# Performance work log

Measured on AMD Instinct MI355X. Metric: run time of the kernel, lower is better.

Reference implementation:

```python
import jax, jax.numpy as jnp
import numpy as np

N = 20000      # nodes
E = 320000     # edges (avg degree 16)
D = 128        # emb_dim
L = 5          # num_layer
NV = 119       # node vocab (atom types)
EV = 5         # edge vocab (bond types)
BN_EPS = 1e-5


def setup_inputs() -> dict:
    key = jax.random.key(0)
    ks = jax.random.split(key, 8)
    s = 0.1
    return {
        "x": jax.random.randint(ks[0], (N,), 0, NV),
        "edge_index": jax.random.randint(ks[1], (2, E), 0, N),
        "edge_attr": jax.random.randint(ks[2], (E,), 0, EV),
        "node_emb1": jax.random.normal(ks[3], (NV, D), jnp.float32) * s,
        "node_emb2": jax.random.normal(ks[4], (NV, D), jnp.float32) * s,
        "edge_emb": jax.random.normal(ks[5], (2, L, EV, D), jnp.float32) * s,
        "eps": jnp.zeros((2, L), jnp.float32),
        "W": jax.random.normal(ks[6], (2, L, D, D), jnp.float32) / np.sqrt(D).astype(np.float32),
        "b": jnp.zeros((2, L, D), jnp.float32),
        "bn_gamma": jnp.ones((2, L, D), jnp.float32),
        "bn_beta": jnp.zeros((2, L, D), jnp.float32),
        "cross_unit": jnp.full((L, 2, 2), 0.5, jnp.float32),
    }


def gin_conv(h, src, dst, eattr, edge_tab, eps, W, b):
    # message: relu(x_j + edge_embedding), aggregated by add at target nodes
    msg = jax.nn.relu(h[src] + edge_tab[eattr])            # [E, D]
    agg = jax.ops.segment_sum(msg, dst, num_segments=h.shape[0])  # [N, D]
    return ((1.0 + eps) * h + agg) @ W.T + b               # mlp = single Linear


def batch_norm(h, gamma, beta):
    # training-mode BatchNorm1d over the node dimension (biased variance)
    mu = h.mean(axis=0)
    var = h.var(axis=0)
    return (h - mu) * jax.lax.rsqrt(var + BN_EPS) * gamma + beta


def reference(x, edge_index, edge_attr, node_emb1, node_emb2, edge_emb, eps, W, b,
              bn_gamma, bn_beta, cross_unit):
    src, dst = edge_index[0], edge_index[1]
    h1 = node_emb1[x]   # NodeEncoder tower 1
    h2 = node_emb2[x]   # NodeEncoder tower 2
    for l in range(L):
        a1 = gin_conv(h1, src, dst, edge_attr, edge_emb[0, l], eps[0, l], W[0, l], b[0, l])
        a1 = batch_norm(a1, bn_gamma[0, l], bn_beta[0, l])
        a2 = gin_conv(h2, src, dst, edge_attr, edge_emb[1, l], eps[1, l], W[1, l], b[1, l])
        a2 = batch_norm(a2, bn_gamma[1, l], bn_beta[1, l])
        if l < L - 1:
            a1 = jax.nn.relu(a1)
            a2 = jax.nn.relu(a2)
        # dropout: identity (eval mode / deterministic reference)
        # cross-stitch; note h_2 uses the UPDATED h_1 (faithful to source)
        c = cross_unit[l]
        n1 = c[0, 0] * a1 + c[0, 1] * a2
        n2 = c[1, 0] * n1 + c[1, 1] * a2
        h1, h2 = n1, n2
    return (h1, h2)  # JK == 'last'
```

## Files before the change

kernel.cpp:

```cpp
#include <hip/hip_runtime.h>

#define NN 20000
#define EE 320000
#define DD 128
#define LL 5
#define EVV 5
#define BNEPS 1e-5f
#define NB 313
#define EMB_BLOCKS 2500
#define CVT_BLOCKS 160
#define CNT_BLOCKS 1250

typedef __attribute__((ext_vector_type(8))) short bf8_t;
typedef __attribute__((ext_vector_type(4))) float f4_t;
typedef __attribute__((ext_vector_type(8))) unsigned short us8;

__device__ inline unsigned short f2bf(float f) {
    union { float f; unsigned u; } v;
    v.f = f;
    unsigned r = v.u + 0x7fffu + ((v.u >> 16) & 1u);
    return (unsigned short)(r >> 16);
}
__device__ inline float bf2f(unsigned short h) {
    union { unsigned u; float f; } v;
    v.u = ((unsigned)h) << 16;
    return v.f;
}
__device__ inline float4 bf2f4(ushort4 u) {
    float4 f;
    f.x = bf2f(u.x); f.y = bf2f(u.y); f.z = bf2f(u.z); f.w = bf2f(u.w);
    return f;
}
__device__ inline float4 add4(float4 a, float4 b) {
    float4 r;
    r.x = a.x + b.x; r.y = a.y + b.y; r.z = a.z + b.z; r.w = a.w + b.w;
    return r;
}

__device__ inline void xform4(float4 v1, float4 v2,
                              float4 s1, float4 t1, float4 s2, float4 t2,
                              float c00, float c01, float c10, float c11,
                              int dorelu, float4& n1, float4& n2) {
    float x1, x2, m1, m2;
#define XE(f)                                                    \
    x1 = v1.f * s1.f + t1.f;                                     \
    x2 = v2.f * s2.f + t2.f;                                     \
    x1 = dorelu ? fmaxf(x1, 0.f) : x1;                           \
    x2 = dorelu ? fmaxf(x2, 0.f) : x2;                           \
    m1 = c00 * x1 + c01 * x2;                                    \
    m2 = c10 * m1 + c11 * x2;                                    \
    n1.f = m1;                                                   \
    n2.f = m2;
    XE(x) XE(y) XE(z) XE(w)
#undef XE
}

__device__ inline void bn_coeffs(const float* __restrict__ statsL,
                                 const float* __restrict__ gall,
                                 const float* __restrict__ btall,
                                 int pl, int c,
                                 float4& s1, float4& t1, float4& s2, float4& t2) {
    const float inv = 1.0f / (float)NN;
    int ch = c * 4;
#define BNC(tw, sv, tv)                                                       \
    {                                                                         \
        const float* gp = gall + (size_t)((tw) * LL + pl) * DD + ch;          \
        const float* bp = btall + (size_t)((tw) * LL + pl) * DD + ch;         \
        float r[4];                                                           \
        _Pragma("unroll") for (int j = 0; j < 4; j++) {                       \
            float sum = statsL[(tw) * 256 + ch + j];                          \
            float sq = statsL[(tw) * 256 + 128 + ch + j];                     \
            float mu = sum * inv;                                             \
            float var = sq * inv - mu * mu;                                   \
            float rs = rsqrtf(var + BNEPS);                                   \
            float sc = rs * gp[j];                                            \
            r[j] = sc;                                                        \
            ((float*)&tv)[j] = bp[j] - mu * sc;                               \
        }                                                                     \
        sv.x = r[0]; sv.y = r[1]; sv.z = r[2]; sv.w = r[3];                   \
    }
    BNC(0, s1, t1)
    BNC(1, s2, t2)
#undef BNC
}

__device__ inline ushort4 hi4(float4 v) {
    ushort4 h;
    h.x = f2bf(v.x); h.y = f2bf(v.y); h.z = f2bf(v.z); h.w = f2bf(v.w);
    return h;
}
__device__ inline ushort4 lo4(float4 v, ushort4 h) {
    ushort4 l;
    l.x = f2bf(v.x - bf2f(h.x)); l.y = f2bf(v.y - bf2f(h.y));
    l.z = f2bf(v.z - bf2f(h.z)); l.w = f2bf(v.w - bf2f(h.w));
    return l;
}


__global__ __launch_bounds__(256) void prep_kernel(
    const int* __restrict__ x,
    const float4* __restrict__ e1, const float4* __restrict__ e2,
    ushort4* __restrict__ yh, ushort4* __restrict__ yl,
    const float4* __restrict__ Wall,
    ushort4* __restrict__ Wbh, ushort4* __restrict__ Wbl,
    const int* __restrict__ dst, int* __restrict__ deg,
    float* __restrict__ stats,
    const float* __restrict__ etab, unsigned short* __restrict__ etb2) {
    int bid = blockIdx.x;
    int tid = threadIdx.x;
    if (bid < EMB_BLOCKS) {
        int idx = bid * 256 + tid;
        int r = idx >> 5, c = idx & 31;
        int v = x[r];
        float4 w1 = e1[v * 32 + c];
        float4 w2 = e2[v * 32 + c];
        ushort4 h = hi4(w1);
        yh[(size_t)r * 64 + c] = h;
        yl[(size_t)r * 64 + c] = lo4(w1, h);
        h = hi4(w2);
        yh[(size_t)r * 64 + 32 + c] = h;
        yl[(size_t)r * 64 + 32 + c] = lo4(w2, h);
    } else if (bid < EMB_BLOCKS + CVT_BLOCKS) {
        int i = (bid - EMB_BLOCKS) * 256 + tid;
        float4 w = Wall[i];
        ushort4 oh = hi4(w);
        Wbh[i] = oh;
        Wbl[i] = lo4(w, oh);
    } else if (bid < EMB_BLOCKS + CVT_BLOCKS + CNT_BLOCKS) {
        int e = (bid - EMB_BLOCKS - CVT_BLOCKS) * 256 + tid;
        atomicAdd(&deg[dst[e]], 1);
    } else {
#pragma unroll
        for (int i = 0; i < 10; i++) stats[i * 256 + tid] = 0.f;
        for (int idx = tid; idx < 2 * LL * EVV * DD; idx += 256) {
            int ch = idx & 127;
            int tw = (idx >> 7) & 1;
            int la = idx >> 8;
            int a = la % EVV;
            int l = la / EVV;
            etb2[idx] = f2bf(etab[((size_t)(tw * LL + l) * EVV + a) * DD + ch]);
        }
    }
}


__global__ __launch_bounds__(1024) void scan_kernel(const int* __restrict__ deg,
                                                    int* __restrict__ offs,
                                                    int* __restrict__ pos) {
    __shared__ int wsum[16];
    int t = threadIdx.x;
    int lane = t & 63, wv = t >> 6;
    int base = t * 20;
    int loc[20];
    int s = 0;
#pragma unroll
    for (int i = 0; i < 20; i++) {
        int j = base + i;
        int d = (j < NN) ? deg[j] : 0;
        loc[i] = d;
        s += d;
    }
    int incl = s;
#pragma unroll
    for (int o = 1; o < 64; o <<= 1) {
        int v = __shfl_up(incl, o, 64);
        if (lane >= o) incl += v;
    }
    if (lane == 63) wsum[wv] = incl;
    __syncthreads();
    if (t < 16) {
        int v = wsum[t];
        int iv = v;
#pragma unroll
        for (int o = 1; o < 16; o <<= 1) {
            int u = __shfl_up(iv, o, 64);
            if (t >= o) iv += u;
        }
        wsum[t] = iv - v;
    }
    __syncthreads();
    int run = wsum[wv] + (incl - s);
#pragma unroll
    for (int i = 0; i < 20; i++) {
        int j = base + i;
        if (j < NN) {
            offs[j] = run;
            pos[j] = run;
            run += loc[i];
        }
    }
}

__global__ __launch_bounds__(256) void scatter_kernel(const int* __restrict__ src,
                                                      const int* __restrict__ dst,
                                                      const int* __restrict__ eattr,
                                                      int* __restrict__ pos,
                                                      int2* __restrict__ erec) {
    int e = blockIdx.x * 256 + threadIdx.x;
    if (e < EE) {
        int d = dst[e];
        int p = atomicAdd(&pos[d], 1);
        erec[p] = make_int2(src[e], eattr[e]);
    }
}


__global__ __launch_bounds__(256) void xform_kernel(
    const ushort4* __restrict__ yh, const ushort4* __restrict__ yl,
    ushort4* __restrict__ hph, ushort4* __restrict__ hpl,
    const float* __restrict__ statsL,
    const float* __restrict__ gall, const float* __restrict__ btall,
    const float* __restrict__ crossp, int pl) {
    int idx = blockIdx.x * 256 + threadIdx.x;
    int r = idx >> 5, c = idx & 31;
    float4 s1, t1, s2, t2;
    bn_coeffs(statsL, gall, btall, pl, c, s1, t1, s2, t2);
    float c00 = crossp[0], c01 = crossp[1], c10 = crossp[2], c11 = crossp[3];
    float4 v1 = add4(bf2f4(yh[(size_t)r * 64 + c]), bf2f4(yl[(size_t)r * 64 + c]));
    float4 v2 = add4(bf2f4(yh[(size_t)r * 64 + 32 + c]), bf2f4(yl[(size_t)r * 64 + 32 + c]));
    float4 n1, n2;
    xform4(v1, v2, s1, t1, s2, t2, c00, c01, c10, c11, 1, n1, n2);
    ushort4 h = hi4(n1);
    hph[(size_t)r * 64 + c] = h;
    hpl[(size_t)r * 64 + c] = lo4(n1, h);
    h = hi4(n2);
    hph[(size_t)r * 64 + 32 + c] = h;
    hpl[(size_t)r * 64 + 32 + c] = lo4(n2, h);
}


__global__ __launch_bounds__(256) void aggregate_kernel(
    const us8* __restrict__ hph, const us8* __restrict__ hpl,
    const us8* __restrict__ etb2, int layer,
    const int* __restrict__ offs, const int* __restrict__ deg,
    const int2* __restrict__ erec, const float* __restrict__ epsall,
    us8* __restrict__ uo8) {
    int tid = threadIdx.x;
    int node = blockIdx.x * 4 + (tid >> 6);
    int lane = tid & 63;
    int slot = lane >> 5;
    int c = lane & 31;
    const us8* et = etb2 + (size_t)layer * EVV * 32;

    int off = offs[node];
    int dg = deg[node];
    float a[8];
#pragma unroll
    for (int k = 0; k < 8; k++) a[k] = 0.f;

    int i = 0;
    for (; i + 8 <= dg; i += 8) {
        int2 r0 = erec[off + i + slot];
        int2 r1 = erec[off + i + 2 + slot];
        int2 r2 = erec[off + i + 4 + slot];
        int2 r3 = erec[off + i + 6 + slot];
        us8 h0 = hph[(size_t)r0.x * 32 + c];
        us8 h1 = hph[(size_t)r1.x * 32 + c];
        us8 h2 = hph[(size_t)r2.x * 32 + c];
        us8 h3 = hph[(size_t)r3.x * 32 + c];
        us8 e0 = et[r0.y * 32 + c];
        us8 e1 = et[r1.y * 32 + c];
        us8 e2 = et[r2.y * 32 + c];
        us8 e3 = et[r3.y * 32 + c];
#pragma unroll
        for (int k = 0; k < 8; k++) {
            a[k] += fmaxf(bf2f(h0[k]) + bf2f(e0[k]), 0.f);
            a[k] += fmaxf(bf2f(h1[k]) + bf2f(e1[k]), 0.f);
            a[k] += fmaxf(bf2f(h2[k]) + bf2f(e2[k]), 0.f);
            a[k] += fmaxf(bf2f(h3[k]) + bf2f(e3[k]), 0.f);
        }
    }
    for (; i < dg; i += 2) {
        int j = i + slot;
        bool valid = j < dg;
        int e = off + (valid ? j : 0);
        int2 r = erec[e];
        us8 h = hph[(size_t)r.x * 32 + c];
        us8 ev = et[r.y * 32 + c];
        if (valid) {
#pragma unroll
            for (int k = 0; k < 8; k++) a[k] += fmaxf(bf2f(h[k]) + bf2f(ev[k]), 0.f);
        }
    }

#pragma unroll
    for (int k = 0; k < 8; k++) a[k] += __shfl_xor(a[k], 32, 64);

    us8 sh = hph[(size_t)node * 32 + c];
    us8 sl = hpl[(size_t)node * 32 + c];
    float ep = 1.0f + epsall[(c >> 4) * LL + layer];
    us8 uh, ul;
#pragma unroll
    for (int k = 0; k < 8; k++) {
        float u = ep * (bf2f(sh[k]) + bf2f(sl[k])) + a[k];
        unsigned short h = f2bf(u);
        uh[k] = h;
        ul[k] = f2bf(u - bf2f(h));
    }
    uo8[(size_t)node * 64 + slot * 32 + c] = slot ? ul : uh;
}


__global__ __launch_bounds__(256) void gemm_mfma_kernel(
    const unsigned short* __restrict__ ubuf,
    const unsigned short* __restrict__ Wbh, const unsigned short* __restrict__ Wbl,
    const float* __restrict__ ball, int layer,
    unsigned short* __restrict__ yh, unsigned short* __restrict__ yl,
    float* __restrict__ statsL) {
    __shared__ float accS[64 * 4 * 33];
    __shared__ float sP[2][4][DD];
    int tid = threadIdx.x;
    int tower = blockIdx.y;
    const bf8_t* Wh8 = (const bf8_t*)(Wbh + (size_t)(tower * LL + layer) * DD * DD);
    const bf8_t* Wl8 = (const bf8_t*)(Wbl + (size_t)(tower * LL + layer) * DD * DD);
    const float* bias = ball + (size_t)(tower * LL + layer) * DD;
    const bf8_t* u8 = (const bf8_t*)ubuf;

    int wave = tid >> 6, lane = tid & 63;
    int quad = lane >> 4, m = lane & 15;
    int row_base = blockIdx.x * 64 + wave * 16;

    f4_t acc[8];
#pragma unroll
    for (int nt = 0; nt < 8; nt++) {
        acc[nt][0] = 0.f; acc[nt][1] = 0.f; acc[nt][2] = 0.f; acc[nt][3] = 0.f;
    }

    int aidx = (row_base + m) * 64 + tower * 16;
#pragma unroll
    for (int kt = 0; kt < 4; kt++) {
        bf8_t ah = u8[aidx + kt * 4 + quad];
        bf8_t al = u8[aidx + 32 + kt * 4 + quad];
#pragma unroll
        for (int nt = 0; nt < 8; nt++) {
            bf8_t bh = Wh8[(nt * 16 + m) * 16 + kt * 4 + quad];
            bf8_t bl = Wl8[(nt * 16 + m) * 16 + kt * 4 + quad];
            acc[nt] = __builtin_amdgcn_mfma_f32_16x16x32_bf16(ah, bh, acc[nt], 0, 0, 0);
            acc[nt] = __builtin_amdgcn_mfma_f32_16x16x32_bf16(al, bh, acc[nt], 0, 0, 0);
            acc[nt] = __builtin_amdgcn_mfma_f32_16x16x32_bf16(ah, bl, acc[nt], 0, 0, 0);
        }
    }

#pragma unroll
    for (int nt = 0; nt < 8; nt++) {
        int col = nt * 16 + m;
        float bv = bias[col];
        int cg = col >> 5, kk = col & 31;
        float s = 0.f, q = 0.f;
#pragma unroll
        for (int r = 0; r < 4; r++) {
            int lrow = wave * 16 + quad * 4 + r;
            int row = blockIdx.x * 64 + lrow;
            float v = acc[nt][r] + bv;
            accS[(lrow * 4 + cg) * 33 + kk] = v;
            if (row < NN) { s += v; q += v * v; }
        }
        s += __shfl_xor(s, 16, 64); s += __shfl_xor(s, 32, 64);
        q += __shfl_xor(q, 16, 64); q += __shfl_xor(q, 32, 64);
        if (quad == 0) {
            sP[0][wave][col] = s;
            sP[1][wave][col] = q;
        }
    }
    __syncthreads();

    {
        int lrow = tid >> 2, cg = tid & 3;
        int grow = blockIdx.x * 64 + lrow;
        if (grow < NN) {
            const float* srcp = &accS[(lrow * 4 + cg) * 33];
            us8* yhp = (us8*)yh;
            us8* ylp = (us8*)yl;
            size_t base = (size_t)grow * 32 + tower * 16 + cg * 4;
#pragma unroll
            for (int j = 0; j < 4; j++) {
                us8 hv, lv;
#pragma unroll
                for (int k = 0; k < 8; k++) {
                    float v = srcp[j * 8 + k];
                    unsigned short h = f2bf(v);
                    hv[k] = h;
                    lv[k] = f2bf(v - bf2f(h));
                }
                yhp[base + j] = hv;
                ylp[base + j] = lv;
            }
        }
    }

    int ch = tid & 127, sq = tid >> 7;
    float v = sP[sq][0][ch] + sP[sq][1][ch] + sP[sq][2][ch] + sP[sq][3][ch];
    atomicAdd(&statsL[tower * 256 + tid], v);
}


__global__ __launch_bounds__(256) void bn_final_kernel(
    const ushort4* __restrict__ yh, const ushort4* __restrict__ yl,
    float4* __restrict__ o1, float4* __restrict__ o2,
    const float* __restrict__ statsL,
    const float* __restrict__ gall, const float* __restrict__ btall,
    const float* __restrict__ crossp) {
    int idx = blockIdx.x * 256 + threadIdx.x;
    int r = idx >> 5, c = idx & 31;
    float4 s1, t1, s2, t2;
    bn_coeffs(statsL, gall, btall, LL - 1, c, s1, t1, s2, t2);
    float c00 = crossp[0], c01 = crossp[1], c10 = crossp[2], c11 = crossp[3];
    float4 v1 = add4(bf2f4(yh[(size_t)r * 64 + c]), bf2f4(yl[(size_t)r * 64 + c]));
    float4 v2 = add4(bf2f4(yh[(size_t)r * 64 + 32 + c]), bf2f4(yl[(size_t)r * 64 + 32 + c]));
    float4 n1, n2;
    xform4(v1, v2, s1, t1, s2, t2, c00, c01, c10, c11, 0, n1, n2);
    o1[(size_t)r * 32 + c] = n1;
    o2[(size_t)r * 32 + c] = n2;
}


extern "C" void kernel_launch(void* const* d_in, const int* in_sizes, int n_in,
                              void* d_out, int out_size, void* d_ws, size_t ws_size,
                              hipStream_t stream) {
    const int* x = (const int*)d_in[0];
    const int* eidx = (const int*)d_in[1];
    const int* eattr = (const int*)d_in[2];
    const float* emb1 = (const float*)d_in[3];
    const float* emb2 = (const float*)d_in[4];
    const float* etab = (const float*)d_in[5];
    const float* epsv = (const float*)d_in[6];
    const float* Wall = (const float*)d_in[7];
    const float* ball = (const float*)d_in[8];
    const float* gall = (const float*)d_in[9];
    const float* btall = (const float*)d_in[10];
    const float* cross = (const float*)d_in[11];
    float* out = (float*)d_out;

    const size_t ND = (size_t)NN * DD;
    char* p = (char*)d_ws;
    unsigned short* yh = (unsigned short*)p;   p += (size_t)NN * 256 * 2;
    unsigned short* yl = (unsigned short*)p;   p += (size_t)NN * 256 * 2;
    unsigned short* hph = (unsigned short*)p;  p += (size_t)NN * 256 * 2;
    unsigned short* hpl = (unsigned short*)p;  p += (size_t)NN * 256 * 2;
    unsigned short* ubuf = (unsigned short*)p; p += (size_t)NN * 512 * 2;
    unsigned short* Wbh = (unsigned short*)p;  p += (size_t)2 * LL * DD * DD * 2;
    unsigned short* Wbl = (unsigned short*)p;  p += (size_t)2 * LL * DD * DD * 2;
    unsigned short* etb2 = (unsigned short*)p; p += (size_t)2 * LL * EVV * DD * 2;
    int* deg = (int*)p;               p += (size_t)NN * 4;
    int* offs = (int*)p;              p += (size_t)NN * 4;
    int* pos = (int*)p;               p += (size_t)NN * 4;
    int2* erec = (int2*)p;            p += (size_t)EE * 8;
    float* stats = (float*)p;         p += (size_t)LL * 512 * 4;

    const int* src = eidx;
    const int* dst = eidx + EE;

    hipMemsetAsync(deg, 0, (size_t)NN * 4, stream);
    prep_kernel<<<EMB_BLOCKS + CVT_BLOCKS + CNT_BLOCKS + 1, 256, 0, stream>>>(
        x, (const float4*)emb1, (const float4*)emb2,
        (ushort4*)yh, (ushort4*)yl,
        (const float4*)Wall, (ushort4*)Wbh, (ushort4*)Wbl, dst, deg, stats,
        etab, etb2);
    scan_kernel<<<1, 1024, 0, stream>>>(deg, offs, pos);
    scatter_kernel<<<EE / 256, 256, 0, stream>>>(src, dst, eattr, pos, erec);

    for (int l = 0; l < LL; l++) {
        const unsigned short* hsrc_h = yh;
        const unsigned short* hsrc_l = yl;
        if (l > 0) {
            xform_kernel<<<(NN * 32) / 256, 256, 0, stream>>>(
                (const ushort4*)yh, (const ushort4*)yl,
                (ushort4*)hph, (ushort4*)hpl,
                stats + (size_t)(l - 1) * 512, gall, btall,
                cross + (l - 1) * 4, l - 1);
            hsrc_h = hph;
            hsrc_l = hpl;
        }
        aggregate_kernel<<<NN / 4, 256, 0, stream>>>(
            (const us8*)hsrc_h, (const us8*)hsrc_l, (const us8*)etb2, l,
            offs, deg, erec, epsv, (us8*)ubuf);
        dim3 g(NB, 2);
        gemm_mfma_kernel<<<g, 256, 0, stream>>>(ubuf, Wbh, Wbl, ball, l, yh, yl,
                                                stats + (size_t)l * 512);
    }
    bn_final_kernel<<<(NN * 32) / 256, 256, 0, stream>>>(
        (const ushort4*)yh, (const ushort4*)yl, (float4*)out, (float4*)(out + ND),
        stats + (size_t)(LL - 1) * 512, gall, btall, cross + (LL - 1) * 4);
}
```

Measured before the change: 504.5 us.

## Fuse neighbor aggregation into MFMA GEMM via shared-memory staging

Merges the aggregation kernel and the split-bf16 GEMM kernel into one 512-thread kernel. Each block aggregates 64 nodes into an XOR-swizzled shared-memory tile, then eight waves run the MFMA GEMM for both towers and write outputs and BN statistics. This removes the global ubuf round trip and one launch per layer. The cost is only 313 blocks for the gather-heavy aggregation phase, which reduces the parallelism available to hide memory latency, plus more shared memory per block. Separate embedding buffers are added so the fused kernel can write yh/yl while layer 0 reads its input from eh/el.

```diff
diff --git a/kernel.cpp b/kernel.cpp
--- a/kernel.cpp
+++ b/kernel.cpp
@@ -6,7 +6,7 @@
 #define LL 5
 #define EVV 5
 #define BNEPS 1e-5f
-#define NB 313
+#define FB 313
 #define EMB_BLOCKS 2500
 #define CVT_BLOCKS 160
 #define CNT_BLOCKS 1250
@@ -100,7 +100,7 @@
 __global__ __launch_bounds__(256) void prep_kernel(
     const int* __restrict__ x,
     const float4* __restrict__ e1, const float4* __restrict__ e2,
-    ushort4* __restrict__ yh, ushort4* __restrict__ yl,
+    ushort4* __restrict__ eh, ushort4* __restrict__ el,
     const float4* __restrict__ Wall,
     ushort4* __restrict__ Wbh, ushort4* __restrict__ Wbl,
     const int* __restrict__ dst, int* __restrict__ deg,
@@ -115,11 +115,11 @@
         float4 w1 = e1[v * 32 + c];
         float4 w2 = e2[v * 32 + c];
         ushort4 h = hi4(w1);
-        yh[(size_t)r * 64 + c] = h;
-        yl[(size_t)r * 64 + c] = lo4(w1, h);
+        eh[(size_t)r * 64 + c] = h;
+        el[(size_t)r * 64 + c] = lo4(w1, h);
         h = hi4(w2);
-        yh[(size_t)r * 64 + 32 + c] = h;
-        yl[(size_t)r * 64 + 32 + c] = lo4(w2, h);
+        eh[(size_t)r * 64 + 32 + c] = h;
+        el[(size_t)r * 64 + 32 + c] = lo4(w2, h);
     } else if (bid < EMB_BLOCKS + CVT_BLOCKS) {
         int i = (bid - EMB_BLOCKS) * 256 + tid;
         float4 w = Wall[i];
@@ -229,108 +229,114 @@
 }
 
 
-__global__ __launch_bounds__(256) void aggregate_kernel(
+__global__ __launch_bounds__(512, 4) void agg_gemm_kernel(
     const us8* __restrict__ hph, const us8* __restrict__ hpl,
     const us8* __restrict__ etb2, int layer,
     const int* __restrict__ offs, const int* __restrict__ deg,
     const int2* __restrict__ erec, const float* __restrict__ epsall,
-    us8* __restrict__ uo8) {
-    int tid = threadIdx.x;
-    int node = blockIdx.x * 4 + (tid >> 6);
-    int lane = tid & 63;
-    int slot = lane >> 5;
-    int c = lane & 31;
-    const us8* et = etb2 + (size_t)layer * EVV * 32;
-
-    int off = offs[node];
-    int dg = deg[node];
-    float a[8];
-#pragma unroll
-    for (int k = 0; k < 8; k++) a[k] = 0.f;
-
-    int i = 0;
-    for (; i + 8 <= dg; i += 8) {
-        int2 r0 = erec[off + i + slot];
-        int2 r1 = erec[off + i + 2 + slot];
-        int2 r2 = erec[off + i + 4 + slot];
-        int2 r3 = erec[off + i + 6 + slot];
-        us8 h0 = hph[(size_t)r0.x * 32 + c];
-        us8 h1 = hph[(size_t)r1.x * 32 + c];
-        us8 h2 = hph[(size_t)r2.x * 32 + c];
-        us8 h3 = hph[(size_t)r3.x * 32 + c];
-        us8 e0 = et[r0.y * 32 + c];
-        us8 e1 = et[r1.y * 32 + c];
-        us8 e2 = et[r2.y * 32 + c];
-        us8 e3 = et[r3.y * 32 + c];
-#pragma unroll
-        for (int k = 0; k < 8; k++) {
-            a[k] += fmaxf(bf2f(h0[k]) + bf2f(e0[k]), 0.f);
-            a[k] += fmaxf(bf2f(h1[k]) + bf2f(e1[k]), 0.f);
-            a[k] += fmaxf(bf2f(h2[k]) + bf2f(e2[k]), 0.f);
-            a[k] += fmaxf(bf2f(h3[k]) + bf2f(e3[k]), 0.f);
-        }
-    }
-    for (; i < dg; i += 2) {
-        int j = i + slot;
-        bool valid = j < dg;
-        int e = off + (valid ? j : 0);
-        int2 r = erec[e];
-        us8 h = hph[(size_t)r.x * 32 + c];
-        us8 ev = et[r.y * 32 + c];
-        if (valid) {
-#pragma unroll
-            for (int k = 0; k < 8; k++) a[k] += fmaxf(bf2f(h[k]) + bf2f(ev[k]), 0.f);
-        }
-    }
-
-#pragma unroll
-    for (int k = 0; k < 8; k++) a[k] += __shfl_xor(a[k], 32, 64);
-
-    us8 sh = hph[(size_t)node * 32 + c];
-    us8 sl = hpl[(size_t)node * 32 + c];
-    float ep = 1.0f + epsall[(c >> 4) * LL + layer];
-    us8 uh, ul;
-#pragma unroll
-    for (int k = 0; k < 8; k++) {
-        float u = ep * (bf2f(sh[k]) + bf2f(sl[k])) + a[k];
-        unsigned short h = f2bf(u);
-        uh[k] = h;
-        ul[k] = f2bf(u - bf2f(h));
-    }
-    uo8[(size_t)node * 64 + slot * 32 + c] = slot ? ul : uh;
-}
-
-
-__global__ __launch_bounds__(256) void gemm_mfma_kernel(
-    const unsigned short* __restrict__ ubuf,
     const unsigned short* __restrict__ Wbh, const unsigned short* __restrict__ Wbl,
-    const float* __restrict__ ball, int layer,
+    const float* __restrict__ ball,
     unsigned short* __restrict__ yh, unsigned short* __restrict__ yl,
     float* __restrict__ statsL) {
-    __shared__ float accS[64 * 4 * 33];
-    __shared__ float sP[2][4][DD];
+    __shared__ float accS[2 * 64 * 4 * 33];
+    __shared__ float sP[2][2][4][DD];
+    us8* uS = (us8*)accS;
+
     int tid = threadIdx.x;
-    int tower = blockIdx.y;
+    int w = tid >> 6, lane = tid & 63;
+
+    {
+        int slot = lane >> 5;
+        int c = lane & 31;
+        const us8* et = etb2 + (size_t)layer * EVV * 32;
+        float ep = 1.0f + epsall[(c >> 4) * LL + layer];
+#pragma unroll 1
+        for (int rnd = 0; rnd < 8; rnd++) {
+            int row = w * 8 + rnd;
+            int node = blockIdx.x * 64 + row;
+            us8 outv;
+            if (node < NN) {
+                int off = offs[node];
+                int dg = deg[node];
+                float a[8];
+#pragma unroll
+                for (int k = 0; k < 8; k++) a[k] = 0.f;
+                int i = 0;
+                for (; i + 8 <= dg; i += 8) {
+                    int2 r0 = erec[off + i + slot];
+                    int2 r1 = erec[off + i + 2 + slot];
+                    int2 r2 = erec[off + i + 4 + slot];
+                    int2 r3 = erec[off + i + 6 + slot];
+                    us8 h0 = hph[(size_t)r0.x * 32 + c];
+                    us8 h1 = hph[(size_t)r1.x * 32 + c];
+                    us8 h2 = hph[(size_t)r2.x * 32 + c];
+                    us8 h3 = hph[(size_t)r3.x * 32 + c];
+                    us8 e0 = et[r0.y * 32 + c];
+                    us8 e1 = et[r1.y * 32 + c];
+                    us8 e2 = et[r2.y * 32 + c];
+                    us8 e3 = et[r3.y * 32 + c];
+#pragma unroll
+                    for (int k = 0; k < 8; k++) {
+                        a[k] += fmaxf(bf2f(h0[k]) + bf2f(e0[k]), 0.f);
+                        a[k] += fmaxf(bf2f(h1[k]) + bf2f(e1[k]), 0.f);
+                        a[k] += fmaxf(bf2f(h2[k]) + bf2f(e2[k]), 0.f);
+                        a[k] += fmaxf(bf2f(h3[k]) + bf2f(e3[k]), 0.f);
+                    }
+                }
+                for (; i < dg; i += 2) {
+                    int j = i + slot;
+                    bool valid = j < dg;
+                    int e = off + (valid ? j : 0);
+                    int2 r = erec[e];
+                    us8 h = hph[(size_t)r.x * 32 + c];
+                    us8 ev = et[r.y * 32 + c];
+                    if (valid) {
+#pragma unroll
+                        for (int k = 0; k < 8; k++)
+                            a[k] += fmaxf(bf2f(h[k]) + bf2f(ev[k]), 0.f);
+                    }
+                }
+#pragma unroll
+                for (int k = 0; k < 8; k++) a[k] += __shfl_xor(a[k], 32, 64);
+                us8 sh = hph[(size_t)node * 32 + c];
+                us8 sl = hpl[(size_t)node * 32 + c];
+                us8 uh, ul;
+#pragma unroll
+                for (int k = 0; k < 8; k++) {
+                    float u = ep * (bf2f(sh[k]) + bf2f(sl[k])) + a[k];
+                    unsigned short h = f2bf(u);
+                    uh[k] = h;
+                    ul[k] = f2bf(u - bf2f(h));
+                }
+                outv = slot ? ul : uh;
+            } else {
+#pragma unroll
+                for (int k = 0; k < 8; k++) outv[k] = 0;
+            }
+            int unit = slot * 32 + c;
+            uS[row * 64 + (unit ^ (row & 7))] = outv;
+        }
+    }
+    __syncthreads();
+
+    int tower = w & 1, rt = w >> 1;
+    int quad = lane >> 4, m = lane & 15;
     const bf8_t* Wh8 = (const bf8_t*)(Wbh + (size_t)(tower * LL + layer) * DD * DD);
     const bf8_t* Wl8 = (const bf8_t*)(Wbl + (size_t)(tower * LL + layer) * DD * DD);
     const float* bias = ball + (size_t)(tower * LL + layer) * DD;
-    const bf8_t* u8 = (const bf8_t*)ubuf;
-
-    int wave = tid >> 6, lane = tid & 63;
-    int quad = lane >> 4, m = lane & 15;
-    int row_base = blockIdx.x * 64 + wave * 16;
+    const bf8_t* u8 = (const bf8_t*)uS;
 
     f4_t acc[8];
 #pragma unroll
     for (int nt = 0; nt < 8; nt++) {
         acc[nt][0] = 0.f; acc[nt][1] = 0.f; acc[nt][2] = 0.f; acc[nt][3] = 0.f;
     }
-
-    int aidx = (row_base + m) * 64 + tower * 16;
+    int lrow = rt * 16 + m;
+    int sw = lrow & 7;
 #pragma unroll
     for (int kt = 0; kt < 4; kt++) {
-        bf8_t ah = u8[aidx + kt * 4 + quad];
-        bf8_t al = u8[aidx + 32 + kt * 4 + quad];
+        bf8_t ah = u8[lrow * 64 + ((tower * 16 + kt * 4 + quad) ^ sw)];
+        bf8_t al = u8[lrow * 64 + ((tower * 16 + 32 + kt * 4 + quad) ^ sw)];
 #pragma unroll
         for (int nt = 0; nt < 8; nt++) {
             bf8_t bh = Wh8[(nt * 16 + m) * 16 + kt * 4 + quad];
@@ -340,7 +346,9 @@
             acc[nt] = __builtin_amdgcn_mfma_f32_16x16x32_bf16(ah, bl, acc[nt], 0, 0, 0);
         }
     }
-
+    __syncthreads();
+
+    float* aS = accS + tower * (64 * 4 * 33);
 #pragma unroll
     for (int nt = 0; nt < 8; nt++) {
         int col = nt * 16 + m;
@@ -349,29 +357,30 @@
         float s = 0.f, q = 0.f;
 #pragma unroll
         for (int r = 0; r < 4; r++) {
-            int lrow = wave * 16 + quad * 4 + r;
-            int row = blockIdx.x * 64 + lrow;
+            int lr2 = rt * 16 + quad * 4 + r;
+            int row = blockIdx.x * 64 + lr2;
             float v = acc[nt][r] + bv;
-            accS[(lrow * 4 + cg) * 33 + kk] = v;
+            aS[(lr2 * 4 + cg) * 33 + kk] = v;
             if (row < NN) { s += v; q += v * v; }
         }
         s += __shfl_xor(s, 16, 64); s += __shfl_xor(s, 32, 64);
         q += __shfl_xor(q, 16, 64); q += __shfl_xor(q, 32, 64);
         if (quad == 0) {
-            sP[0][wave][col] = s;
-            sP[1][wave][col] = q;
+            sP[tower][0][rt][col] = s;
+            sP[tower][1][rt][col] = q;
         }
     }
     __syncthreads();
 
     {
-        int lrow = tid >> 2, cg = tid & 3;
-        int grow = blockIdx.x * 64 + lrow;
+        int lr = tid >> 3, g = tid & 7;
+        int tw = g >> 2, cg = g & 3;
+        int grow = blockIdx.x * 64 + lr;
         if (grow < NN) {
-            const float* srcp = &accS[(lrow * 4 + cg) * 33];
+            const float* srcp = accS + tw * (64 * 4 * 33) + (lr * 4 + cg) * 33;
             us8* yhp = (us8*)yh;
             us8* ylp = (us8*)yl;
-            size_t base = (size_t)grow * 32 + tower * 16 + cg * 4;
+            size_t base = (size_t)grow * 32 + tw * 16 + cg * 4;
 #pragma unroll
             for (int j = 0; j < 4; j++) {
                 us8 hv, lv;
@@ -388,9 +397,12 @@
         }
     }
 
-    int ch = tid & 127, sq = tid >> 7;
-    float v = sP[sq][0][ch] + sP[sq][1][ch] + sP[sq][2][ch] + sP[sq][3][ch];
-    atomicAdd(&statsL[tower * 256 + tid], v);
+    {
+        int tw = tid >> 8, idx = tid & 255;
+        int sq = idx >> 7, ch = idx & 127;
+        float v = sP[tw][sq][0][ch] + sP[tw][sq][1][ch] + sP[tw][sq][2][ch] + sP[tw][sq][3][ch];
+        atomicAdd(&statsL[tw * 256 + idx], v);
+    }
 }
 
 
@@ -437,7 +449,8 @@
     unsigned short* yl = (unsigned short*)p;   p += (size_t)NN * 256 * 2;
     unsigned short* hph = (unsigned short*)p;  p += (size_t)NN * 256 * 2;
     unsigned short* hpl = (unsigned short*)p;  p += (size_t)NN * 256 * 2;
-    unsigned short* ubuf = (unsigned short*)p; p += (size_t)NN * 512 * 2;
+    unsigned short* eh = (unsigned short*)p;   p += (size_t)NN * 256 * 2;
+    unsigned short* el = (unsigned short*)p;   p += (size_t)NN * 256 * 2;
     unsigned short* Wbh = (unsigned short*)p;  p += (size_t)2 * LL * DD * DD * 2;
     unsigned short* Wbl = (unsigned short*)p;  p += (size_t)2 * LL * DD * DD * 2;
     unsigned short* etb2 = (unsigned short*)p; p += (size_t)2 * LL * EVV * DD * 2;
@@ -453,15 +466,15 @@
     hipMemsetAsync(deg, 0, (size_t)NN * 4, stream);
     prep_kernel<<<EMB_BLOCKS + CVT_BLOCKS + CNT_BLOCKS + 1, 256, 0, stream>>>(
         x, (const float4*)emb1, (const float4*)emb2,
-        (ushort4*)yh, (ushort4*)yl,
+        (ushort4*)eh, (ushort4*)el,
         (const float4*)Wall, (ushort4*)Wbh, (ushort4*)Wbl, dst, deg, stats,
         etab, etb2);
     scan_kernel<<<1, 1024, 0, stream>>>(deg, offs, pos);
     scatter_kernel<<<EE / 256, 256, 0, stream>>>(src, dst, eattr, pos, erec);
 
     for (int l = 0; l < LL; l++) {
-        const unsigned short* hsrc_h = yh;
-        const unsigned short* hsrc_l = yl;
+        const unsigned short* hsrc_h = eh;
+        const unsigned short* hsrc_l = el;
         if (l > 0) {
             xform_kernel<<<(NN * 32) / 256, 256, 0, stream>>>(
                 (const ushort4*)yh, (const ushort4*)yl,
@@ -471,12 +484,10 @@
             hsrc_h = hph;
             hsrc_l = hpl;
         }
-        aggregate_kernel<<<NN / 4, 256, 0, stream>>>(
+        agg_gemm_kernel<<<FB, 512, 0, stream>>>(
             (const us8*)hsrc_h, (const us8*)hsrc_l, (const us8*)etb2, l,
-            offs, deg, erec, epsv, (us8*)ubuf);
-        dim3 g(NB, 2);
-        gemm_mfma_kernel<<<g, 256, 0, stream>>>(ubuf, Wbh, Wbl, ball, l, yh, yl,
-                                                stats + (size_t)l * 512);
+            offs, deg, erec, epsv, Wbh, Wbl, ball, yh, yl,
+            stats + (size_t)l * 512);
     }
     bn_final_kernel<<<(NN * 32) / 256, 256, 0, stream>>>(
         (const ushort4*)yh, (const ushort4*)yl, (float4*)out, (float4*)(out + ND),
```

After: 585.6 us. 16.1% more time.
